# Optimization experiments

Hardware: AMD Instinct MI355X
Metric: run time of the kernel (lower is better)

## Reference

```python
import jax, jax.numpy as jnp
import numpy as np

B, S, HID = 2, 2048, 1024
NH, HD = 16, 64  # num heads, head dim
NEG = 1e10

def setup_inputs() -> dict:
    key = jax.random.key(0)
    ks = jax.random.split(key, 4)
    scale = 1.0 / np.sqrt(HID)
    return {
        "hidden_states": jax.random.normal(ks[0], (B, S, HID), jnp.float32),
        "attention_mask": jnp.zeros((B, 1, 1, S), jnp.float32),
        "Wq": jax.random.normal(ks[1], (HID, HID), jnp.float32) * scale,
        "bq": jnp.zeros((HID,), jnp.float32),
        "Wk": jax.random.normal(ks[2], (HID, HID), jnp.float32) * scale,
        "bk": jnp.zeros((HID,), jnp.float32),
        "Wv": jax.random.normal(ks[3], (HID, HID), jnp.float32) * scale,
        "bv": jnp.zeros((HID,), jnp.float32),
    }

def _split_heads(x):
    # [B,S,HID] -> [B,NH,S,HD]
    return x.reshape(B, S, NH, HD).transpose(0, 2, 1, 3)

def reference(hidden_states, attention_mask, Wq, bq, Wk, bk, Wv, bv):
    q = _split_heads(hidden_states @ Wq.T + bq)
    k = _split_heads(hidden_states @ Wk.T + bk)
    v = _split_heads(hidden_states @ Wv.T + bv)
    scores = jnp.einsum("bhqd,bhkd->bhqk", q, k) / np.sqrt(HD)
    causal = jnp.tril(jnp.ones((S, S), jnp.float32))  # [S,S]
    scores = scores * causal - NEG * (1.0 - causal)
    scores = scores + attention_mask
    probs = jax.nn.softmax(scores, axis=-1)  # [B,NH,S,S]
    ctx = jnp.einsum("bhqk,bhkd->bhqd", probs, v)
    ctx = ctx.transpose(0, 2, 1, 3).reshape(B, S, HID)
    return (ctx, probs)
```

## Files before the change

kernel.cpp:

```cpp
#include <hip/hip_runtime.h>

#define S_LEN 2048
#define HIDN  1024
#define NHEAD 16
#define HDIM  64
#define NBATCH 2

typedef __bf16 bf16x8 __attribute__((ext_vector_type(8)));
typedef float  f32x4  __attribute__((ext_vector_type(4)));
typedef unsigned short u16;
typedef unsigned short u16x4 __attribute__((ext_vector_type(4)));

__device__ __forceinline__ u16 f2bf(float f) {
    union { float f; unsigned int u; } v; v.f = f;
    unsigned int u = v.u;
    unsigned int r = ((u >> 16) & 1u) + 0x7FFFu;
    return (u16)((u + r) >> 16);
}

__device__ __forceinline__ f32x4 mfma16(bf16x8 a, bf16x8 b, f32x4 c) {
    return __builtin_amdgcn_mfma_f32_16x16x32_bf16(a, b, c, 0, 0, 0);
}

__device__ __forceinline__ f32x4 zf4() { f32x4 z = {0.f, 0.f, 0.f, 0.f}; return z; }

__device__ __forceinline__ void gld16(void* lds, const void* g) {
    __builtin_amdgcn_global_load_lds(
        (const __attribute__((address_space(1))) void*)g,
        (__attribute__((address_space(3))) void*)lds, 16, 0, 0);
}

__global__ __launch_bounds__(256) void cvt_bf16(
    const float* __restrict__ s, u16* __restrict__ d, int n)
{
    int i = (blockIdx.x * 256 + threadIdx.x) * 4;
    if (i >= n) return;
    float4 v = *(const float4*)&s[i];
    u16x4 o = { f2bf(v.x), f2bf(v.y), f2bf(v.z), f2bf(v.w) };
    *(u16x4*)&d[i] = o;
}

__global__ __launch_bounds__(256) void qkv_gemm(
    const u16* __restrict__ hsb,
    const u16* __restrict__ Wqb, const u16* __restrict__ Wkb, const u16* __restrict__ Wvb,
    const float* __restrict__ bq, const float* __restrict__ bk, const float* __restrict__ bv,
    u16* __restrict__ Qf, u16* __restrict__ Kf, u16* __restrict__ Vt)
{
    __shared__ u16 As[128 * 32];
    __shared__ u16 Bs[128 * 32];

    const int z = blockIdx.z;
    const u16*   __restrict__ W    = (z == 0) ? Wqb : (z == 1) ? Wkb : Wvb;
    const float* __restrict__ bias = (z == 0) ? bq  : (z == 1) ? bk  : bv;

    const int mbase = blockIdx.x * 128;
    const int nbase = blockIdx.y * 128;
    const int tid  = threadIdx.x;
    const int lane = tid & 63;
    const int wv   = tid >> 6;
    const int wrow = wv >> 1, wcol = wv & 1;
    const int lrow = lane & 15, quad = lane >> 4;

    const int c0 = tid, c1 = tid + 256;
    const int r0 = c0 >> 2, o0 = (c0 & 3) * 8;
    const int r1 = c1 >> 2, o1 = (c1 & 3) * 8;
    const u16* a0p = &hsb[(size_t)(mbase + r0) * HIDN + o0];
    const u16* a1p = &hsb[(size_t)(mbase + r1) * HIDN + o1];
    const u16* b0p = &W  [(size_t)(nbase + r0) * HIDN + o0];
    const u16* b1p = &W  [(size_t)(nbase + r1) * HIDN + o1];

    f32x4 acc[4][4];
#pragma unroll
    for (int i = 0; i < 4; ++i)
#pragma unroll
        for (int j = 0; j < 4; ++j) acc[i][j] = zf4();

    for (int k0 = 0; k0 < HIDN; k0 += 32) {
        gld16(&As[c0 * 8], a0p + k0);
        gld16(&As[c1 * 8], a1p + k0);
        gld16(&Bs[c0 * 8], b0p + k0);
        gld16(&Bs[c1 * 8], b1p + k0);
        __syncthreads();

        bf16x8 af[4], bfr[4];
#pragma unroll
        for (int i = 0; i < 4; ++i)
            af[i] = *(const bf16x8*)&As[(wrow * 64 + i * 16 + lrow) * 32 + quad * 8];
#pragma unroll
        for (int j = 0; j < 4; ++j)
            bfr[j] = *(const bf16x8*)&Bs[(wcol * 64 + j * 16 + lrow) * 32 + quad * 8];
#pragma unroll
        for (int i = 0; i < 4; ++i)
#pragma unroll
            for (int j = 0; j < 4; ++j)
                acc[i][j] = mfma16(af[i], bfr[j], acc[i][j]);
        __syncthreads();
    }

    if (z == 2) {
        const int bb = mbase >> 11;
        const int sb = mbase & 2047;
#pragma unroll
        for (int i = 0; i < 4; ++i) {
#pragma unroll
            for (int j = 0; j < 4; ++j) {
                const int n = nbase + wcol * 64 + j * 16 + lrow;
                const int hh = n >> 6, d = n & 63;
                const float bs = bias[n];
                const int sbase = sb + wrow * 64 + i * 16 + quad * 4;
                u16x4 pk = { f2bf(acc[i][j][0] + bs), f2bf(acc[i][j][1] + bs),
                             f2bf(acc[i][j][2] + bs), f2bf(acc[i][j][3] + bs) };
                *(u16x4*)&Vt[(((size_t)(bb * NHEAD + hh)) * HDIM + d) * S_LEN + sbase] = pk;
            }
        }
    } else {
        u16* __restrict__ O = (z == 0) ? Qf : Kf;
#pragma unroll
        for (int i = 0; i < 4; ++i) {
#pragma unroll
            for (int j = 0; j < 4; ++j) {
                const int n = nbase + wcol * 64 + j * 16 + lrow;
                const float bs = bias[n];
#pragma unroll
                for (int reg = 0; reg < 4; ++reg) {
                    const int m = mbase + wrow * 64 + i * 16 + quad * 4 + reg;
                    O[(size_t)m * HIDN + n] = f2bf(acc[i][j][reg] + bs);
                }
            }
        }
    }
}

__global__ __launch_bounds__(256) void attn_kernel(
    const u16* __restrict__ Qf,
    const u16* __restrict__ Kf,
    const u16* __restrict__ Vt,
    const float* __restrict__ amask,
    float* __restrict__ ctx,
    float* __restrict__ probs)
{
    const int qt = blockIdx.x;
    const int h  = blockIdx.y;
    const int b  = blockIdx.z;
    const int bh = b * NHEAD + h;
    const int tid  = threadIdx.x;
    const int lane = tid & 63;
    const int wv   = tid >> 6;
    const int lrow = lane & 15, quad = lane >> 4;
    const int row0 = qt * 16;
    const int nkt  = (qt >> 2) + 1;

    __shared__ u16   plds[4][16 * 64];
    __shared__ float cxs[4][64 * 17];
    __shared__ float l_sh[4][16];

    {
        const int tail  = nkt * 64;
        const int nt4   = (S_LEN - tail) >> 2;
        const int r  = tid >> 4;
        const int c0 = tid & 15;
        const f32x4 zf = {0.f, 0.f, 0.f, 0.f};
        float* pr = &probs[((size_t)bh * S_LEN + row0 + r) * S_LEN + tail];
        for (int c4 = c0; c4 < nt4; c4 += 16)
            __builtin_nontemporal_store(zf, (f32x4*)&pr[c4 * 4]);
    }

    const u16* qp = &Qf[((size_t)b * S_LEN + row0 + lrow) * HIDN + h * HDIM + quad * 8];
    const bf16x8 qa0 = *(const bf16x8*)qp;
    const bf16x8 qa1 = *(const bf16x8*)(qp + 32);

    float l_lane[4] = {0.f, 0.f, 0.f, 0.f};
    for (int kt = wv; kt < nkt; kt += 4) {
        f32x4 c[4];
#pragma unroll
        for (int cb = 0; cb < 4; ++cb) {
            const int col = kt * 64 + cb * 16 + lrow;
            const u16* kp = &Kf[((size_t)b * S_LEN + col) * HIDN + h * HDIM + quad * 8];
            bf16x8 kb0 = *(const bf16x8*)kp;
            bf16x8 kb1 = *(const bf16x8*)(kp + 32);
            c[cb] = mfma16(qa0, kb0, zf4());
            c[cb] = mfma16(qa1, kb1, c[cb]);
        }
#pragma unroll
        for (int cb = 0; cb < 4; ++cb) {
            const int col = kt * 64 + cb * 16 + lrow;
            const float mv = amask[b * S_LEN + col];
#pragma unroll
            for (int reg = 0; reg < 4; ++reg) {
                const int row = row0 + quad * 4 + reg;
                const float e = __expf(c[cb][reg] * 0.125f + mv - 8.0f);
                l_lane[reg] += (col <= row) ? e : 0.f;
            }
        }
    }
#pragma unroll
    for (int reg = 0; reg < 4; ++reg) {
#pragma unroll
        for (int off = 1; off < 16; off <<= 1)
            l_lane[reg] += __shfl_xor(l_lane[reg], off, 16);
    }
    if (lrow == 0) {
#pragma unroll
        for (int reg = 0; reg < 4; ++reg)
            l_sh[wv][quad * 4 + reg] = l_lane[reg];
    }
    __syncthreads();
    float inv_l[4];
#pragma unroll
    for (int reg = 0; reg < 4; ++reg) {
        const int rr = quad * 4 + reg;
        inv_l[reg] = 1.f / (l_sh[0][rr] + l_sh[1][rr] + l_sh[2][rr] + l_sh[3][rr]);
    }

    f32x4 av[4];
#pragma unroll
    for (int db = 0; db < 4; ++db) av[db] = zf4();

    for (int kt = wv; kt < nkt; kt += 4) {
        f32x4 c[4];
#pragma unroll
        for (int cb = 0; cb < 4; ++cb) {
            const int col = kt * 64 + cb * 16 + lrow;
            const u16* kp = &Kf[((size_t)b * S_LEN + col) * HIDN + h * HDIM + quad * 8];
            bf16x8 kb0 = *(const bf16x8*)kp;
            bf16x8 kb1 = *(const bf16x8*)(kp + 32);
            c[cb] = mfma16(qa0, kb0, zf4());
            c[cb] = mfma16(qa1, kb1, c[cb]);
        }
#pragma unroll
        for (int cb = 0; cb < 4; ++cb) {
            const int col = kt * 64 + cb * 16 + lrow;
            const float mv = amask[b * S_LEN + col];
#pragma unroll
            for (int reg = 0; reg < 4; ++reg) {
                const int row = row0 + quad * 4 + reg;
                const float p = (col <= row)
                    ? __expf(c[cb][reg] * 0.125f + mv - 8.0f) * inv_l[reg] : 0.f;
                __builtin_nontemporal_store(p, &probs[((size_t)bh * S_LEN + row) * S_LEN + col]);
                plds[wv][(quad * 4 + reg) * 64 + cb * 16 + lrow] = f2bf(p);
            }
        }
        bf16x8 pa0 = *(const bf16x8*)&plds[wv][lrow * 64 + quad * 8];
        bf16x8 pa1 = *(const bf16x8*)&plds[wv][lrow * 64 + 32 + quad * 8];
#pragma unroll
        for (int db = 0; db < 4; ++db) {
            const u16* vp = &Vt[((size_t)bh * HDIM + db * 16 + lrow) * S_LEN + kt * 64 + quad * 8];
            bf16x8 vb0 = *(const bf16x8*)vp;
            bf16x8 vb1 = *(const bf16x8*)(vp + 32);
            av[db] = mfma16(pa0, vb0, av[db]);
            av[db] = mfma16(pa1, vb1, av[db]);
        }
    }

#pragma unroll
    for (int db = 0; db < 4; ++db)
#pragma unroll
        for (int reg = 0; reg < 4; ++reg)
            cxs[wv][lane * 17 + db * 4 + reg] = av[db][reg];
    __syncthreads();
#pragma unroll
    for (int reg = 0; reg < 4; ++reg) {
        const int idx = lane * 17 + wv * 4 + reg;
        const float s = cxs[0][idx] + cxs[1][idx] + cxs[2][idx] + cxs[3][idx];
        __builtin_nontemporal_store(
            s, &ctx[((size_t)b * S_LEN + row0 + quad * 4 + reg) * HIDN + h * HDIM + wv * 16 + lrow]);
    }
}

extern "C" void kernel_launch(void* const* d_in, const int* in_sizes, int n_in,
                              void* d_out, int out_size, void* d_ws, size_t ws_size,
                              hipStream_t stream)
{
    const float* hs    = (const float*)d_in[0];
    const float* amask = (const float*)d_in[1];
    const float* Wq    = (const float*)d_in[2];
    const float* bq    = (const float*)d_in[3];
    const float* Wk    = (const float*)d_in[4];
    const float* bk    = (const float*)d_in[5];
    const float* Wv    = (const float*)d_in[6];
    const float* bv    = (const float*)d_in[7];

    float* out   = (float*)d_out;
    float* ctx   = out;
    float* probs = out + (size_t)NBATCH * S_LEN * HIDN;

    const size_t NTOK = (size_t)NBATCH * S_LEN;
    u16* hsb = (u16*)d_ws;
    u16* Wqb = hsb + NTOK * HIDN;
    u16* Wkb = Wqb + (size_t)HIDN * HIDN;
    u16* Wvb = Wkb + (size_t)HIDN * HIDN;
    u16* Qf  = Wvb + (size_t)HIDN * HIDN;
    u16* Kf  = Qf + NTOK * HIDN;
    u16* Vt  = Kf + NTOK * HIDN;

    const int n_hs = (int)(NTOK * HIDN);
    const int n_w  = HIDN * HIDN;
    cvt_bf16<<<n_hs / 1024, 256, 0, stream>>>(hs, hsb, n_hs);
    cvt_bf16<<<n_w  / 1024, 256, 0, stream>>>(Wq, Wqb, n_w);
    cvt_bf16<<<n_w  / 1024, 256, 0, stream>>>(Wk, Wkb, n_w);
    cvt_bf16<<<n_w  / 1024, 256, 0, stream>>>(Wv, Wvb, n_w);

    qkv_gemm<<<dim3(32, 8, 3), 256, 0, stream>>>(hsb, Wqb, Wkb, Wvb, bq, bk, bv, Qf, Kf, Vt);
    attn_kernel<<<dim3(128, 16, 2), 256, 0, stream>>>(Qf, Kf, Vt, amask, ctx, probs);
}
```

Measured before the change: 782.7 us.

## Stage probs through LDS for vectorized stores, reverse tile order, specialize diagonal tile

Probability tiles are now written to LDS as fp32 and read back row-contiguously, so the probs matrix is stored with 16-byte nontemporal vector stores instead of scattered scalar stores. The bf16 MFMA operands are built from the same LDS tile by truncating packs, which replaces round-to-nearest conversion. Query tiles are scheduled in reverse so the longest causal rows start first, and only the diagonal key tile keeps the causal mask test. Costs are double the LDS for the staging buffer, an extra LDS round trip, and slightly different rounding of P for the PV product.

```diff
diff --git a/kernel.cpp b/kernel.cpp
--- a/kernel.cpp
+++ b/kernel.cpp
@@ -8,6 +8,7 @@
 
 typedef __bf16 bf16x8 __attribute__((ext_vector_type(8)));
 typedef float  f32x4  __attribute__((ext_vector_type(4)));
+typedef unsigned int  u32x4 __attribute__((ext_vector_type(4)));
 typedef unsigned short u16;
 typedef unsigned short u16x4 __attribute__((ext_vector_type(4)));
 
@@ -23,6 +24,17 @@
 }
 
 __device__ __forceinline__ f32x4 zf4() { f32x4 z = {0.f, 0.f, 0.f, 0.f}; return z; }
+
+__device__ __forceinline__ bf16x8 pack8_trunc(f32x4 a, f32x4 b) {
+    union { f32x4 f; u32x4 u; } ua, ub;
+    ua.f = a; ub.f = b;
+    union { unsigned int d[4]; bf16x8 v; } r;
+    r.d[0] = __builtin_amdgcn_perm(ua.u.y, ua.u.x, 0x07060302u);
+    r.d[1] = __builtin_amdgcn_perm(ua.u.w, ua.u.z, 0x07060302u);
+    r.d[2] = __builtin_amdgcn_perm(ub.u.y, ub.u.x, 0x07060302u);
+    r.d[3] = __builtin_amdgcn_perm(ub.u.w, ub.u.z, 0x07060302u);
+    return r.v;
+}
 
 __device__ __forceinline__ void gld16(void* lds, const void* g) {
     __builtin_amdgcn_global_load_lds(
@@ -139,7 +151,7 @@
     float* __restrict__ ctx,
     float* __restrict__ probs)
 {
-    const int qt = blockIdx.x;
+    const int qt = 127 - blockIdx.x;
     const int h  = blockIdx.y;
     const int b  = blockIdx.z;
     const int bh = b * NHEAD + h;
@@ -148,9 +160,10 @@
     const int wv   = tid >> 6;
     const int lrow = lane & 15, quad = lane >> 4;
     const int row0 = qt * 16;
-    const int nkt  = (qt >> 2) + 1;
-
-    __shared__ u16   plds[4][16 * 64];
+    const int dti  = qt >> 2;
+    const int nkt  = dti + 1;
+
+    __shared__ float pfl[4][16 * 64];
     __shared__ float cxs[4][64 * 17];
     __shared__ float l_sh[4][16];
 
@@ -181,15 +194,26 @@
             c[cb] = mfma16(qa0, kb0, zf4());
             c[cb] = mfma16(qa1, kb1, c[cb]);
         }
-#pragma unroll
-        for (int cb = 0; cb < 4; ++cb) {
-            const int col = kt * 64 + cb * 16 + lrow;
-            const float mv = amask[b * S_LEN + col];
-#pragma unroll
-            for (int reg = 0; reg < 4; ++reg) {
-                const int row = row0 + quad * 4 + reg;
-                const float e = __expf(c[cb][reg] * 0.125f + mv - 8.0f);
-                l_lane[reg] += (col <= row) ? e : 0.f;
+        if (kt == dti) {
+#pragma unroll
+            for (int cb = 0; cb < 4; ++cb) {
+                const int col = kt * 64 + cb * 16 + lrow;
+                const float m8 = amask[b * S_LEN + col] - 8.0f;
+#pragma unroll
+                for (int reg = 0; reg < 4; ++reg) {
+                    const int row = row0 + quad * 4 + reg;
+                    const float e = __expf(fmaf(c[cb][reg], 0.125f, m8));
+                    l_lane[reg] += (col <= row) ? e : 0.f;
+                }
+            }
+        } else {
+#pragma unroll
+            for (int cb = 0; cb < 4; ++cb) {
+                const int col = kt * 64 + cb * 16 + lrow;
+                const float m8 = amask[b * S_LEN + col] - 8.0f;
+#pragma unroll
+                for (int reg = 0; reg < 4; ++reg)
+                    l_lane[reg] += __expf(fmaf(c[cb][reg], 0.125f, m8));
             }
         }
     }
@@ -227,21 +251,47 @@
             c[cb] = mfma16(qa0, kb0, zf4());
             c[cb] = mfma16(qa1, kb1, c[cb]);
         }
-#pragma unroll
-        for (int cb = 0; cb < 4; ++cb) {
-            const int col = kt * 64 + cb * 16 + lrow;
-            const float mv = amask[b * S_LEN + col];
-#pragma unroll
-            for (int reg = 0; reg < 4; ++reg) {
-                const int row = row0 + quad * 4 + reg;
-                const float p = (col <= row)
-                    ? __expf(c[cb][reg] * 0.125f + mv - 8.0f) * inv_l[reg] : 0.f;
-                __builtin_nontemporal_store(p, &probs[((size_t)bh * S_LEN + row) * S_LEN + col]);
-                plds[wv][(quad * 4 + reg) * 64 + cb * 16 + lrow] = f2bf(p);
-            }
-        }
-        bf16x8 pa0 = *(const bf16x8*)&plds[wv][lrow * 64 + quad * 8];
-        bf16x8 pa1 = *(const bf16x8*)&plds[wv][lrow * 64 + 32 + quad * 8];
+        if (kt == dti) {
+#pragma unroll
+            for (int cb = 0; cb < 4; ++cb) {
+                const int col = kt * 64 + cb * 16 + lrow;
+                const float m8 = amask[b * S_LEN + col] - 8.0f;
+#pragma unroll
+                for (int reg = 0; reg < 4; ++reg) {
+                    const int row = row0 + quad * 4 + reg;
+                    const float p = (col <= row)
+                        ? __expf(fmaf(c[cb][reg], 0.125f, m8)) * inv_l[reg] : 0.f;
+                    pfl[wv][(quad * 4 + reg) * 64 + cb * 16 + lrow] = p;
+                }
+            }
+        } else {
+#pragma unroll
+            for (int cb = 0; cb < 4; ++cb) {
+                const int col = kt * 64 + cb * 16 + lrow;
+                const float m8 = amask[b * S_LEN + col] - 8.0f;
+#pragma unroll
+                for (int reg = 0; reg < 4; ++reg) {
+                    const float p = __expf(fmaf(c[cb][reg], 0.125f, m8)) * inv_l[reg];
+                    pfl[wv][(quad * 4 + reg) * 64 + cb * 16 + lrow] = p;
+                }
+            }
+        }
+
+#pragma unroll
+        for (int it = 0; it < 4; ++it) {
+            const int r  = it * 4 + quad;
+            const int f4 = lrow;
+            f32x4 v = *(const f32x4*)&pfl[wv][r * 64 + f4 * 4];
+            __builtin_nontemporal_store(
+                v, (f32x4*)&probs[((size_t)bh * S_LEN + row0 + r) * S_LEN + kt * 64 + f4 * 4]);
+        }
+
+        f32x4 p0 = *(const f32x4*)&pfl[wv][lrow * 64 + quad * 8];
+        f32x4 p1 = *(const f32x4*)&pfl[wv][lrow * 64 + quad * 8 + 4];
+        f32x4 p2 = *(const f32x4*)&pfl[wv][lrow * 64 + 32 + quad * 8];
+        f32x4 p3 = *(const f32x4*)&pfl[wv][lrow * 64 + 32 + quad * 8 + 4];
+        bf16x8 pa0 = pack8_trunc(p0, p1);
+        bf16x8 pa1 = pack8_trunc(p2, p3);
 #pragma unroll
         for (int db = 0; db < 4; ++db) {
             const u16* vp = &Vt[((size_t)bh * HDIM + db * 16 + lrow) * S_LEN + kt * 64 + quad * 8];
```

After: 775.0 us. About the same (-1.0%).
